# Kernel tuning notes

Hardware: AMD Instinct MI355X
Metric: run time of the kernel (lower is better)

Reference implementation:

```python
import jax, jax.numpy as jnp
import numpy as np

B, C, RES, N_ANGLES = 32, 16, 128, 64


def setup_inputs() -> dict:
    key = jax.random.key(0)
    k1, k2, k3 = jax.random.split(key, 3)
    x = jax.random.normal(k1, (B, C, RES, RES), dtype=jnp.float32)
    # torch-radon setup: angles = np.linspace(0, 2*pi, 64)
    angles = jnp.linspace(0.0, 2.0 * np.pi, N_ANGLES).astype(jnp.float32)
    # Conv2d(16, 1, 1) params (kaiming-ish scale)
    conv_w = jax.random.normal(k2, (1, C, 1, 1), dtype=jnp.float32) * (1.0 / np.sqrt(C))
    conv_b = jax.random.normal(k3, (1,), dtype=jnp.float32) * 0.01
    return {"x": x, "angles": angles, "conv_w": conv_w, "conv_b": conv_b}


def _radon(x, angles):
    # x: (B, C, H, W) -> sinogram (B, C, n_angles, det_count)
    H = x.shape[-2]
    W = x.shape[-1]
    center = (H - 1) / 2.0
    # detector positions s and ray-integration positions t, in pixel units, centered
    coords = jnp.arange(H, dtype=jnp.float32) - center  # (RES,)

    def proj_one(carry, theta):
        c, s = jnp.cos(theta), jnp.sin(theta)
        # rotated sampling grid: (D, T) = (detector, along-ray)
        xs = coords[:, None] * c - coords[None, :] * s + center
        ys = coords[:, None] * s + coords[None, :] * c + center
        x0 = jnp.floor(xs)
        y0 = jnp.floor(ys)
        wx = xs - x0  # bilinear weights
        wy = ys - y0
        x0i = x0.astype(jnp.int32)
        y0i = y0.astype(jnp.int32)

        def g(yi, xi):
            # zero-padded gather: (B, C, D, T)
            valid = ((yi >= 0) & (yi < H) & (xi >= 0) & (xi < W)).astype(x.dtype)
            v = x[:, :, jnp.clip(yi, 0, H - 1), jnp.clip(xi, 0, W - 1)]
            return v * valid

        val = (g(y0i, x0i) * ((1.0 - wy) * (1.0 - wx))
               + g(y0i, x0i + 1) * ((1.0 - wy) * wx)
               + g(y0i + 1, x0i) * (wy * (1.0 - wx))
               + g(y0i + 1, x0i + 1) * (wy * wx))
        # line integral: sum along the ray (T axis) -> (B, C, D)
        return carry, val.sum(axis=-1)

    _, sino = jax.lax.scan(proj_one, 0, angles)  # (A, B, C, D)
    return jnp.transpose(sino, (1, 2, 0, 3))      # (B, C, A, D)


def reference(x, angles, conv_w, conv_b):
    sino = _radon(x, angles)  # (B, C, A, D)
    # 1x1 conv: contract channel dim
    out = jnp.einsum('bcad,oc->boad', sino, conv_w[:, :, 0, 0])
    return out + conv_b[None, :, None, None]
```

## Files before the change

kernel.cpp:

```cpp
#include <hip/hip_runtime.h>


#define B_    32
#define C_    16
#define RES   128
#define NA    64
#define SLDS  133
#define ROWS  132
#define NELEM (ROWS * SLDS)
#define NPAD  18432
#define NPAIR 16

typedef _Float16 half2v __attribute__((ext_vector_type(2)));

__global__ __launch_bounds__(256) void chanpack(const float* __restrict__ x,
                                                const float* __restrict__ w,
                                                uint2* __restrict__ pk) {
    const int blk = blockIdx.x;
    const int p   = blk >> 7;
    const int q   = blk & 127;
    const int t   = threadIdx.x;
    const int u   = t >> 7;
    const int m   = t & 127;

    __shared__ float rowbuf[2][130];

    float wr[C_];
#pragma unroll
    for (int c = 0; c < C_; ++c) wr[c] = w[c];

    const float* xb = x + ((size_t)(2 * p + u) * C_) * (RES * RES) + q * RES + m;
    float acc = 0.f;
#pragma unroll
    for (int c = 0; c < C_; ++c) acc = fmaf(wr[c], xb[c * (RES * RES)], acc);

    rowbuf[u][m + 1] = acc;
    if (m == 0) { rowbuf[u][0] = 0.f; rowbuf[u][129] = 0.f; }
    __syncthreads();

    uint2* dst = pk + (size_t)p * NPAD + (q + 2) * SLDS;
    if (t < SLDS) {
        int c = t;
        uint2 v = make_uint2(0u, 0u);
        if (c >= 1 && c <= 129) {
            v.x = __builtin_bit_cast(unsigned int,
                      __builtin_amdgcn_cvt_pkrtz(rowbuf[0][c - 1], rowbuf[0][c]));
            v.y = __builtin_bit_cast(unsigned int,
                      __builtin_amdgcn_cvt_pkrtz(rowbuf[1][c - 1], rowbuf[1][c]));
        }
        dst[c] = v;
    }

    if (q == 0) {
        uint2* base = pk + (size_t)p * NPAD;
        const uint2 z = make_uint2(0u, 0u);
        for (int k = t; k < 2 * SLDS; k += 256) {
            base[k] = z;
            base[130 * SLDS + k] = z;
        }
        for (int k = t; k < NPAD - NELEM; k += 256)
            base[NELEM + k] = z;
    }
}

__global__ __launch_bounds__(512) void radon_k(const uint2* __restrict__ pk,
                                               const float* __restrict__ angles,
                                               const float* __restrict__ bias,
                                               float* __restrict__ out) {
    __shared__ uint2 lds[NPAD];
    const int bid = blockIdx.x;
    const int p   = bid >> 4;
    const int grp = bid & 15;
    const int t   = threadIdx.x;

    {
        const uint4* src = (const uint4*)(pk + (size_t)p * NPAD);
        uint4*       dst = (uint4*)lds;
#pragma unroll
        for (int k = 0; k < 18; ++k) dst[k * 512 + t] = src[k * 512 + t];
    }
    __syncthreads();

    const int a = (t >> 7) * 16 + grp;
    const int i = t & 127;
    float th = angles[a];
    float s, c;
    __sincosf(th, &s, &c);

    const float ci = (float)i - 63.5f;
    const float Xb = fmaf(ci, c, fmaf(63.5f, s, 65.5f));
    const float Yb = fmaf(ci, s, fmaf(-63.5f, c, 65.5f));
    const float ns = -s;

    const half2v kM1P1 = half2v{(_Float16)(-1.f), (_Float16)(1.f)};
    const half2v kP1Z  = half2v{(_Float16)( 1.f), (_Float16)(0.f)};

    auto addr_of = [&](float jf) -> int {
        float X  = fmaf(jf, ns, Xb);
        float Y  = fmaf(jf, c,  Yb);
        float gx = fminf(fmaxf(floorf(X), 0.f), 130.f);
        float gy = fminf(fmaxf(floorf(Y), 0.f), 130.f);
        return (int)fmaf(gy, (float)SLDS, gx);
    };

    float acc00 = 0.f, acc01 = 0.f, acc10 = 0.f, acc11 = 0.f;

    int   addr = addr_of(0.f);
    uint2 q0 = lds[addr];
    uint2 q1 = lds[addr + SLDS];

#pragma unroll 8
    for (int j = 0; j < RES; ++j) {
        float jf = (float)j;
        float X  = fmaf(jf, ns, Xb);
        float Y  = fmaf(jf, c,  Yb);
        float wx = X - floorf(X);
        float wy = Y - floorf(Y);

        uint2 q0n, q1n;
        if (j < RES - 1) {
            int an = addr_of(jf + 1.f);
            q0n = lds[an];
            q1n = lds[an + SLDS];
        }

        half2v hwx = __builtin_bit_cast(half2v, __builtin_amdgcn_cvt_pkrtz(wx, wx));
        half2v hwy = __builtin_bit_cast(half2v, __builtin_amdgcn_cvt_pkrtz(wy, wy));
        half2v uwx = __builtin_elementwise_fma(hwx, kM1P1, kP1Z);
        half2v uwy = __builtin_elementwise_fma(hwy, kM1P1, kP1Z);
        half2v wa  = uwx * __builtin_shufflevector(uwy, uwy, 0, 0);
        half2v wb  = uwx * __builtin_shufflevector(uwy, uwy, 1, 1);

        acc00 = __builtin_amdgcn_fdot2(__builtin_bit_cast(half2v, q0.x), wa, acc00, false);
        acc10 = __builtin_amdgcn_fdot2(__builtin_bit_cast(half2v, q0.y), wa, acc10, false);
        acc01 = __builtin_amdgcn_fdot2(__builtin_bit_cast(half2v, q1.x), wb, acc01, false);
        acc11 = __builtin_amdgcn_fdot2(__builtin_bit_cast(half2v, q1.y), wb, acc11, false);

        q0 = q0n; q1 = q1n;
    }

    float bv = bias[0];
    out[(2 * p)     * (NA * RES) + a * RES + i] = (acc00 + acc01) + bv;
    out[(2 * p + 1) * (NA * RES) + a * RES + i] = (acc10 + acc11) + bv;
}

extern "C" void kernel_launch(void* const* d_in, const int* in_sizes, int n_in,
                              void* d_out, int out_size, void* d_ws, size_t ws_size,
                              hipStream_t stream) {
    const float* x      = (const float*)d_in[0];
    const float* angles = (const float*)d_in[1];
    const float* w      = (const float*)d_in[2];
    const float* bias   = (const float*)d_in[3];
    float* out = (float*)d_out;

    uint2* pk = (uint2*)d_ws;

    chanpack<<<dim3(NPAIR * RES), dim3(256), 0, stream>>>(x, w, pk);
    radon_k<<<dim3(NPAIR * 16), dim3(512), 0, stream>>>(pk, angles, bias, out);
}
```

Before: 97.22 us.

## Vectorize chanpack loads to float4 over 4 rows and streamline radon inner loop

The channel-contraction pack kernel now has each thread load float4 values and handle four rows per block, so it launches a quarter as many blocks with wider, coalesced global loads. The radon kernel issues the angle and bias loads before the LDS fill and moves the barrier after the sincos setup, so that latency overlaps the copy. The inner loop carries the address and fp16 weights for the next step and drops the per-iteration guard and recomputation. The last iteration now does an unconditional, clamped extra LDS read, which is in bounds but wasted work.

```diff
diff --git a/kernel.cpp b/kernel.cpp
--- a/kernel.cpp
+++ b/kernel.cpp
@@ -17,41 +17,66 @@
                                                 const float* __restrict__ w,
                                                 uint2* __restrict__ pk) {
     const int blk = blockIdx.x;
-    const int p   = blk >> 7;
-    const int q   = blk & 127;
+    const int p   = blk >> 5;
+    const int qq  = blk & 31;
     const int t   = threadIdx.x;
     const int u   = t >> 7;
-    const int m   = t & 127;
+    const int v   = (t >> 5) & 3;
+    const int g   = t & 31;
 
-    __shared__ float rowbuf[2][130];
+    __shared__ float rowbuf[2][4][130];
 
-    float wr[C_];
+    const float* xb = x + ((size_t)(2 * p + u) * C_) * (RES * RES)
+                        + (4 * qq + v) * RES + 4 * g;
+    float ax = 0.f, ay = 0.f, az = 0.f, aw = 0.f;
 #pragma unroll
-    for (int c = 0; c < C_; ++c) wr[c] = w[c];
-
-    const float* xb = x + ((size_t)(2 * p + u) * C_) * (RES * RES) + q * RES + m;
-    float acc = 0.f;
-#pragma unroll
-    for (int c = 0; c < C_; ++c) acc = fmaf(wr[c], xb[c * (RES * RES)], acc);
-
-    rowbuf[u][m + 1] = acc;
-    if (m == 0) { rowbuf[u][0] = 0.f; rowbuf[u][129] = 0.f; }
+    for (int c = 0; c < C_; ++c) {
+        const float wc = w[c];
+        const float4 xv = *reinterpret_cast<const float4*>(xb + c * (RES * RES));
+        ax = fmaf(wc, xv.x, ax);
+        ay = fmaf(wc, xv.y, ay);
+        az = fmaf(wc, xv.z, az);
+        aw = fmaf(wc, xv.w, aw);
+    }
+    {
+        float* rb = &rowbuf[u][v][0];
+        rb[4 * g + 1] = ax;
+        rb[4 * g + 2] = ay;
+        rb[4 * g + 3] = az;
+        rb[4 * g + 4] = aw;
+        if (g == 0) { rb[0] = 0.f; rb[129] = 0.f; }
+    }
     __syncthreads();
 
-    uint2* dst = pk + (size_t)p * NPAD + (q + 2) * SLDS;
-    if (t < SLDS) {
-        int c = t;
-        uint2 v = make_uint2(0u, 0u);
-        if (c >= 1 && c <= 129) {
-            v.x = __builtin_bit_cast(unsigned int,
-                      __builtin_amdgcn_cvt_pkrtz(rowbuf[0][c - 1], rowbuf[0][c]));
-            v.y = __builtin_bit_cast(unsigned int,
-                      __builtin_amdgcn_cvt_pkrtz(rowbuf[1][c - 1], rowbuf[1][c]));
+    uint2* dst = pk + (size_t)p * NPAD + (4 * qq + 2) * SLDS;
+
+#pragma unroll
+    for (int pass = 0; pass < 2; ++pass) {
+        const int v2 = 2 * pass + (t >> 7);
+        const int c  = t & 127;
+        uint2 val = make_uint2(0u, 0u);
+        if (c >= 1) {
+            val.x = __builtin_bit_cast(unsigned int,
+                        __builtin_amdgcn_cvt_pkrtz(rowbuf[0][v2][c - 1], rowbuf[0][v2][c]));
+            val.y = __builtin_bit_cast(unsigned int,
+                        __builtin_amdgcn_cvt_pkrtz(rowbuf[1][v2][c - 1], rowbuf[1][v2][c]));
         }
-        dst[c] = v;
+        dst[v2 * SLDS + c] = val;
+    }
+    if (t < 20) {
+        const int v2 = t / 5;
+        const int c  = 128 + t % 5;
+        uint2 val = make_uint2(0u, 0u);
+        if (c <= 129) {
+            val.x = __builtin_bit_cast(unsigned int,
+                        __builtin_amdgcn_cvt_pkrtz(rowbuf[0][v2][c - 1], rowbuf[0][v2][c]));
+            val.y = __builtin_bit_cast(unsigned int,
+                        __builtin_amdgcn_cvt_pkrtz(rowbuf[1][v2][c - 1], rowbuf[1][v2][c]));
+        }
+        dst[v2 * SLDS + c] = val;
     }
 
-    if (q == 0) {
+    if (qq == 0) {
         uint2* base = pk + (size_t)p * NPAD;
         const uint2 z = make_uint2(0u, 0u);
         for (int k = t; k < 2 * SLDS; k += 256) {
@@ -73,20 +98,20 @@
     const int grp = bid & 15;
     const int t   = threadIdx.x;
 
+    const int a = (t >> 7) * 16 + grp;
+    const int i = t & 127;
+    const float th = angles[a];
+    const float bv = bias[0];
+
     {
         const uint4* src = (const uint4*)(pk + (size_t)p * NPAD);
         uint4*       dst = (uint4*)lds;
 #pragma unroll
         for (int k = 0; k < 18; ++k) dst[k * 512 + t] = src[k * 512 + t];
     }
-    __syncthreads();
 
-    const int a = (t >> 7) * 16 + grp;
-    const int i = t & 127;
-    float th = angles[a];
     float s, c;
     __sincosf(th, &s, &c);
-
     const float ci = (float)i - 63.5f;
     const float Xb = fmaf(ci, c, fmaf(63.5f, s, 65.5f));
     const float Yb = fmaf(ci, s, fmaf(-63.5f, c, 65.5f));
@@ -95,51 +120,54 @@
     const half2v kM1P1 = half2v{(_Float16)(-1.f), (_Float16)(1.f)};
     const half2v kP1Z  = half2v{(_Float16)( 1.f), (_Float16)(0.f)};
 
-    auto addr_of = [&](float jf) -> int {
-        float X  = fmaf(jf, ns, Xb);
-        float Y  = fmaf(jf, c,  Yb);
-        float gx = fminf(fmaxf(floorf(X), 0.f), 130.f);
-        float gy = fminf(fmaxf(floorf(Y), 0.f), 130.f);
-        return (int)fmaf(gy, (float)SLDS, gx);
-    };
+    __syncthreads();
 
-    float acc00 = 0.f, acc01 = 0.f, acc10 = 0.f, acc11 = 0.f;
-
-    int   addr = addr_of(0.f);
+    int    addr;
+    half2v hwx, hwy;
+    {
+        const float X  = Xb;
+        const float Y  = Yb;
+        const float fx = floorf(X), fy = floorf(Y);
+        const float gx = fminf(fmaxf(fx, 0.f), 130.f);
+        const float gy = fminf(fmaxf(fy, 0.f), 130.f);
+        addr = (int)fmaf(gy, (float)SLDS, gx);
+        hwx  = __builtin_bit_cast(half2v, __builtin_amdgcn_cvt_pkrtz(X - fx, X - fx));
+        hwy  = __builtin_bit_cast(half2v, __builtin_amdgcn_cvt_pkrtz(Y - fy, Y - fy));
+    }
     uint2 q0 = lds[addr];
     uint2 q1 = lds[addr + SLDS];
 
+    float acc00 = 0.f, acc01 = 0.f, acc10 = 0.f, acc11 = 0.f;
+    float jf = 1.f;
+
 #pragma unroll 8
     for (int j = 0; j < RES; ++j) {
-        float jf = (float)j;
-        float X  = fmaf(jf, ns, Xb);
-        float Y  = fmaf(jf, c,  Yb);
-        float wx = X - floorf(X);
-        float wy = Y - floorf(Y);
+        const float X  = fmaf(jf, ns, Xb);
+        const float Y  = fmaf(jf, c,  Yb);
+        const float fx = floorf(X), fy = floorf(Y);
+        const float wx = X - fx,    wy = Y - fy;
+        const float gx = fminf(fmaxf(fx, 0.f), 130.f);
+        const float gy = fminf(fmaxf(fy, 0.f), 130.f);
+        const int addrn = (int)fmaf(gy, (float)SLDS, gx);
+        const half2v hwxn = __builtin_bit_cast(half2v, __builtin_amdgcn_cvt_pkrtz(wx, wx));
+        const half2v hwyn = __builtin_bit_cast(half2v, __builtin_amdgcn_cvt_pkrtz(wy, wy));
+        const uint2 q0n = lds[addrn];
+        const uint2 q1n = lds[addrn + SLDS];
 
-        uint2 q0n, q1n;
-        if (j < RES - 1) {
-            int an = addr_of(jf + 1.f);
-            q0n = lds[an];
-            q1n = lds[an + SLDS];
-        }
-
-        half2v hwx = __builtin_bit_cast(half2v, __builtin_amdgcn_cvt_pkrtz(wx, wx));
-        half2v hwy = __builtin_bit_cast(half2v, __builtin_amdgcn_cvt_pkrtz(wy, wy));
-        half2v uwx = __builtin_elementwise_fma(hwx, kM1P1, kP1Z);
-        half2v uwy = __builtin_elementwise_fma(hwy, kM1P1, kP1Z);
-        half2v wa  = uwx * __builtin_shufflevector(uwy, uwy, 0, 0);
-        half2v wb  = uwx * __builtin_shufflevector(uwy, uwy, 1, 1);
+        const half2v uwx = __builtin_elementwise_fma(hwx, kM1P1, kP1Z);
+        const half2v uwy = __builtin_elementwise_fma(hwy, kM1P1, kP1Z);
+        const half2v wa  = uwx * __builtin_shufflevector(uwy, uwy, 0, 0);
+        const half2v wb  = uwx * __builtin_shufflevector(uwy, uwy, 1, 1);
 
         acc00 = __builtin_amdgcn_fdot2(__builtin_bit_cast(half2v, q0.x), wa, acc00, false);
         acc10 = __builtin_amdgcn_fdot2(__builtin_bit_cast(half2v, q0.y), wa, acc10, false);
         acc01 = __builtin_amdgcn_fdot2(__builtin_bit_cast(half2v, q1.x), wb, acc01, false);
         acc11 = __builtin_amdgcn_fdot2(__builtin_bit_cast(half2v, q1.y), wb, acc11, false);
 
-        q0 = q0n; q1 = q1n;
+        addr = addrn; hwx = hwxn; hwy = hwyn; q0 = q0n; q1 = q1n;
+        jf += 1.f;
     }
 
-    float bv = bias[0];
     out[(2 * p)     * (NA * RES) + a * RES + i] = (acc00 + acc01) + bv;
     out[(2 * p + 1) * (NA * RES) + a * RES + i] = (acc10 + acc11) + bv;
 }
@@ -155,6 +183,6 @@
 
     uint2* pk = (uint2*)d_ws;
 
-    chanpack<<<dim3(NPAIR * RES), dim3(256), 0, stream>>>(x, w, pk);
+    chanpack<<<dim3(NPAIR * 32), dim3(256), 0, stream>>>(x, w, pk);
     radon_k<<<dim3(NPAIR * 16), dim3(512), 0, stream>>>(pk, angles, bias, out);
 }
```

Result: no change. 96.13 us (-1.1%).
